# Kernel optimization log

Hardware: AMD Instinct MI355X
Metric: run time of the kernel (lower is better)

Reference implementation:

```python
import jax, jax.numpy as jnp
import numpy as np

EPS = 1e-5  # BatchNorm1d default eps


def gcn_conv(x, src, dst, w, b, n):
    # src/dst already include self-loops. Symmetric normalization D^-1/2 (A+I) D^-1/2.
    deg = jnp.zeros((n,), x.dtype).at[dst].add(1.0)
    dinv = jnp.where(deg > 0, jax.lax.rsqrt(jnp.maximum(deg, 1.0)), 0.0)
    norm = dinv[src] * dinv[dst]                      # [E+N]
    h = x @ w                                          # [B, N, H]
    msg = h[:, src, :] * norm[None, :, None]           # gather + scale  [B, E+N, H]
    agg = jnp.zeros_like(h).at[:, dst, :].add(msg)     # scatter-add
    return agg + b


def batch_norm(h, gamma, beta):
    # training-mode BN over the flattened (B*N) axis, biased variance (torch BN forward)
    mu = h.mean(axis=(0, 1))
    var = ((h - mu) ** 2).mean(axis=(0, 1))
    return (h - mu) * jax.lax.rsqrt(var + EPS) * gamma + beta


def reference(x, edge_index, W1, b1, W2, b2, gamma1, beta1, gamma2, beta2, Wc, bc):
    n = x.shape[1]
    loops = jnp.arange(n)
    src = jnp.concatenate([edge_index[0], loops])
    dst = jnp.concatenate([edge_index[1], loops])
    h = jax.nn.relu(gcn_conv(x, src, dst, W1, b1, n))
    h = batch_norm(h, gamma1, beta1)
    # dropout(p=0.2) treated as identity (eval / deterministic reference)
    h = jax.nn.relu(gcn_conv(h, src, dst, W2, b2, n))
    h = batch_norm(h, gamma2, beta2)
    out = (h @ Wc + bc).squeeze(-1)                    # [B, N]
    return out


def setup_inputs() -> dict:
    key = jax.random.key(0)
    ks = jax.random.split(key, 8)
    B, N, E, F, H = 4, 20000, 320000, 64, 128
    s = lambda fan: 1.0 / np.sqrt(fan)
    return {
        "x": jax.random.normal(ks[0], (B, N, F), dtype=jnp.float32),
        "edge_index": jax.random.randint(ks[1], (2, E), 0, N, dtype=jnp.int64),
        "W1": jax.random.normal(ks[2], (F, H), dtype=jnp.float32) * s(F),
        "b1": jnp.zeros((H,), jnp.float32),
        "W2": jax.random.normal(ks[3], (H, H), dtype=jnp.float32) * s(H),
        "b2": jnp.zeros((H,), jnp.float32),
        "gamma1": jnp.ones((H,), jnp.float32),
        "beta1": jnp.zeros((H,), jnp.float32),
        "gamma2": jnp.ones((H,), jnp.float32),
        "beta2": jnp.zeros((H,), jnp.float32),
        "Wc": jax.random.normal(ks[4], (H, 1), dtype=jnp.float32) * s(H),
        "bc": jnp.zeros((1,), jnp.float32),
    }
```

## Files before the change

kernel.cpp:

```cpp
#include <hip/hip_runtime.h>

constexpr int Bb = 4;
constexpr int Nn = 20000;
constexpr int Ff = 64;
constexpr int Hh = 128;
constexpr float BN_EPS = 1e-5f;
constexpr int NSLOTS = 64;
constexpr int NB = (Nn + 1023) / 1024;

typedef __attribute__((ext_vector_type(8))) short bf16x8;
typedef __attribute__((ext_vector_type(4))) float f32x4;

__device__ inline unsigned f2bf(float f) {
    unsigned u = __float_as_uint(f);
    return (u + 0x7fffu + ((u >> 16) & 1u)) >> 16;
}
__device__ inline unsigned pack2(float lo, float hi) { return f2bf(lo) | (f2bf(hi) << 16); }
__device__ inline float bf_lo(unsigned w) { return __uint_as_float(w << 16); }
__device__ inline float bf_hi(unsigned w) { return __uint_as_float(w & 0xffff0000u); }

template <int NU>
__device__ inline void ldrow(unsigned* u, const unsigned* p) {
    if constexpr (NU == 2) { const uint2 t = *(const uint2*)p; u[0] = t.x; u[1] = t.y; }
    else { const uint4 t = *(const uint4*)p; u[0] = t.x; u[1] = t.y; u[2] = t.z; u[3] = t.w; }
}
template <int NU>
__device__ inline void acc_row(float* a, const unsigned* u, float nm) {
#pragma unroll
    for (int c = 0; c < NU; ++c) {
        a[2 * c]     = fmaf(nm, bf_lo(u[c]), a[2 * c]);
        a[2 * c + 1] = fmaf(nm, bf_hi(u[c]), a[2 * c + 1]);
    }
}

__global__ void k_deg(const int* __restrict__ dst, int E, int* __restrict__ deg) {
    int e = blockIdx.x * blockDim.x + threadIdx.x;
    if (e < E) atomicAdd(&deg[dst[e]], 1);
}

__global__ __launch_bounds__(1024) void k_scan1(const int* __restrict__ deg,
                                                int* __restrict__ rowptr,
                                                int* __restrict__ bsum) {
    __shared__ int wsum[16];
    const int tid = threadIdx.x, lane = tid & 63, wid = tid >> 6;
    const int i = blockIdx.x * 1024 + tid;
    const int cnt = (i < Nn) ? (deg[i] + 1) : 0;
    int v = cnt;
#pragma unroll
    for (int d = 1; d < 64; d <<= 1) {
        const int t = __shfl_up(v, d);
        if (lane >= d) v += t;
    }
    if (lane == 63) wsum[wid] = v;
    __syncthreads();
    if (wid == 0) {
        const int orig = (lane < 16) ? wsum[lane] : 0;
        int w = orig;
#pragma unroll
        for (int d = 1; d < 16; d <<= 1) {
            const int t = __shfl_up(w, d);
            if (lane >= d) w += t;
        }
        if (lane == 15) bsum[blockIdx.x] = w;
        if (lane < 16) wsum[lane] = w - orig;
    }
    __syncthreads();
    if (i < Nn) rowptr[i] = wsum[wid] + (v - cnt);
}

__global__ void k_scan2(int* __restrict__ bsum) {
    const int lane = threadIdx.x;
    const int v = (lane < NB) ? bsum[lane] : 0;
    int s = v;
#pragma unroll
    for (int d = 1; d < 64; d <<= 1) {
        const int t = __shfl_up(s, d);
        if (lane >= d) s += t;
    }
    if (lane < NB) bsum[lane] = s - v;
}

__global__ __launch_bounds__(1024) void k_scan3(const int* __restrict__ deg,
                                                int* __restrict__ rowptr,
                                                const int* __restrict__ bsum,
                                                int* __restrict__ cursor,
                                                float* __restrict__ dinv) {
    const int i = blockIdx.x * 1024 + threadIdx.x;
    if (i >= Nn) return;
    const int cnt = deg[i] + 1;
    const int excl = rowptr[i] + bsum[blockIdx.x];
    rowptr[i] = excl;
    cursor[i] = excl;
    dinv[i] = rsqrtf((float)cnt);
    if (i == Nn - 1) rowptr[Nn] = excl + cnt;
}

__global__ void k_fill(const int* __restrict__ src, const int* __restrict__ dst, int E,
                       const float* __restrict__ dinv, int* __restrict__ cursor,
                       int* __restrict__ csr_src, float* __restrict__ csr_norm,
                       float* __restrict__ nsum) {
    int t = blockIdx.x * blockDim.x + threadIdx.x;
    int s, d;
    if (t < E) { s = src[t]; d = dst[t]; }
    else if (t < E + Nn) { s = d = t - E; }
    else return;
    int pos = atomicAdd(&cursor[d], 1);
    const float nm = dinv[s] * dinv[d];
    csr_src[pos]  = s;
    csr_norm[pos] = nm;
    atomicAdd(&nsum[d], nm);
}

__global__ void k_cvt(const float* __restrict__ x, unsigned* __restrict__ xb) {
    const int t = blockIdx.x * 256 + threadIdx.x;
    if (t >= Bb * Nn * 32) return;
    const int c2 = t & 31;
    const int bn = t >> 5;
    const int n  = bn % Nn;
    const int b  = bn / Nn;
    const float2 v = *(const float2*)&x[(size_t)t * 2];
    xb[((size_t)n * Bb + b) * 32 + c2] = pack2(v.x, v.y);
}

__global__ void k_wt1(const float* __restrict__ W, unsigned short* __restrict__ WTf) {
    const int f = blockIdx.x * 256 + threadIdx.x;
    if (f >= 128 * Ff) return;
    const int j = f & 7, lane = (f >> 3) & 63, rest = f >> 9;
    const int ks = rest & 1, tt = rest >> 1;
    const int col = tt * 16 + (lane & 15);
    const int k = ks * 32 + ((lane >> 4) << 3) + j;
    WTf[f] = (unsigned short)f2bf(W[(size_t)k * 128 + col]);
}

__global__ __launch_bounds__(128) void k_prep2(const float* __restrict__ gsum,
                                               const float* __restrict__ gsq,
                                               const float* __restrict__ gamma,
                                               const float* __restrict__ beta,
                                               const float* __restrict__ W2,
                                               unsigned short* __restrict__ WT2f,
                                               float* __restrict__ shW2) {
    __shared__ float sc_s[128], sh_s[128];
    const int c = threadIdx.x;
    float s = 0.f, q = 0.f;
    for (int j = 0; j < NSLOTS; ++j) { s += gsum[j * 128 + c]; q += gsq[j * 128 + c]; }
    const float inv = 1.0f / (float)(Bb * Nn);
    const float mu  = s * inv;
    const float var = q * inv - mu * mu;
    const float sc  = gamma[c] * rsqrtf(var + BN_EPS);
    sc_s[c] = sc;
    sh_s[c] = beta[c] - mu * sc;
    __syncthreads();
    if (blockIdx.x < 64) {
#pragma unroll
        for (int i = 0; i < 2; ++i) {
            const int f = blockIdx.x * 256 + i * 128 + c;
            const int j = f & 7, lane = (f >> 3) & 63, rest = f >> 9;
            const int ks = rest & 3, tt = rest >> 2;
            const int col = tt * 16 + (lane & 15);
            const int k = ks * 32 + ((lane >> 4) << 3) + j;
            WT2f[f] = (unsigned short)f2bf(sc_s[k] * W2[(size_t)k * 128 + col]);
        }
    } else {
        float a = 0.f;
        for (int k = 0; k < 128; ++k) a = fmaf(sh_s[k], W2[(size_t)k * 128 + c], a);
        shW2[c] = a;
    }
}

template <int K, bool L2E>
__global__ __launch_bounds__(64, 6) void k_fmm(const unsigned* __restrict__ G,
                                               const int* __restrict__ rowptr,
                                               const int* __restrict__ csr_src,
                                               const float* __restrict__ csr_norm,
                                               const unsigned short* __restrict__ WTf,
                                               const float* __restrict__ bias,
                                               const float* __restrict__ nsum,
                                               const float* __restrict__ shW2,
                                               unsigned short* __restrict__ Yout,
                                               float* __restrict__ gsum,
                                               float* __restrict__ gsq) {
    constexpr int NKS = K / 32;
    constexpr int AST = K + 8;
    constexpr int NU = K / 32;
    constexpr int ROWU = Bb * K / 2;
    __shared__ alignas(16) unsigned short sA[16 * AST];

    const int lane = threadIdx.x;
    const int cg = lane & 15, kg = lane >> 4;
    const int g = blockIdx.x;
    const int row0 = g * 16;

#pragma unroll
    for (int j = 0; j < 4; ++j) {
        const int v = g * 4 + j;
        const int beg = rowptr[v], end = rowptr[v + 1];
        float a[2 * NU];
#pragma unroll
        for (int c = 0; c < 2 * NU; ++c) a[c] = 0.f;
        int e = beg;
        for (; e + 8 <= end; e += 8) {
            unsigned u[8][NU];
            int si[8];
#pragma unroll
            for (int q = 0; q < 8; ++q) si[q] = csr_src[e + q];
#pragma unroll
            for (int q = 0; q < 8; ++q)
                ldrow<NU>(u[q], G + (size_t)si[q] * ROWU + lane * NU);
#pragma unroll
            for (int q = 0; q < 8; ++q) acc_row<NU>(a, u[q], csr_norm[e + q]);
        }
        for (; e + 4 <= end; e += 4) {
            unsigned u[4][NU];
            int si[4];
#pragma unroll
            for (int q = 0; q < 4; ++q) si[q] = csr_src[e + q];
#pragma unroll
            for (int q = 0; q < 4; ++q)
                ldrow<NU>(u[q], G + (size_t)si[q] * ROWU + lane * NU);
#pragma unroll
            for (int q = 0; q < 4; ++q) acc_row<NU>(a, u[q], csr_norm[e + q]);
        }
        for (; e < end; ++e) {
            unsigned u[NU];
            ldrow<NU>(u, G + (size_t)csr_src[e] * ROWU + lane * NU);
            acc_row<NU>(a, u, csr_norm[e]);
        }
        const int row = j * 4 + kg;
        unsigned p[NU];
#pragma unroll
        for (int c = 0; c < NU; ++c) p[c] = pack2(a[2 * c], a[2 * c + 1]);
        if constexpr (NU == 2) *(uint2*)&sA[row * AST + cg * 4] = *(const uint2*)p;
        else                   *(uint4*)&sA[row * AST + cg * 8] = *(const uint4*)p;
    }

    f32x4 acc[8];
#pragma unroll
    for (int t = 0; t < 8; ++t) acc[t] = (f32x4){0.f, 0.f, 0.f, 0.f};
#pragma unroll
    for (int ks = 0; ks < NKS; ++ks) {
        const bf16x8 av = *(const bf16x8*)&sA[cg * AST + ks * 32 + kg * 8];
#pragma unroll
        for (int t = 0; t < 8; ++t) {
            const bf16x8 bv = *(const bf16x8*)&WTf[(size_t)((t * NKS + ks) * 64 + lane) * 8];
            acc[t] = __builtin_amdgcn_mfma_f32_16x16x32_bf16(av, bv, acc[t], 0, 0, 0);
        }
    }

    const int rbase = kg * 4;
    float ns = 0.f;
    if (L2E) ns = nsum[g * 4 + kg];
    float* gs = gsum + (size_t)(g & (NSLOTS - 1)) * 128;
    float* gq = gsq  + (size_t)(g & (NSLOTS - 1)) * 128;
#pragma unroll
    for (int t = 0; t < 8; ++t) {
        const int col = t * 16 + cg;
        float badd = bias[col];
        if (L2E) badd = fmaf(ns, shW2[col], badd);
        float s = 0.f, q = 0.f;
#pragma unroll
        for (int jj = 0; jj < 4; ++jj) {
            const float y = fmaxf(acc[t][jj] + badd, 0.f);
            Yout[(size_t)(row0 + rbase + jj) * 128 + col] = (unsigned short)f2bf(y);
            s += y; q = fmaf(y, y, q);
        }
        s += __shfl_xor(s, 16); s += __shfl_xor(s, 32);
        q += __shfl_xor(q, 16); q += __shfl_xor(q, 32);
        if (kg == 0) { atomicAdd(&gs[col], s); atomicAdd(&gq[col], q); }
    }
}

__global__ void k_bnfin2(const float* __restrict__ gsum, const float* __restrict__ gsq,
                         const float* __restrict__ gamma, const float* __restrict__ beta,
                         const float* __restrict__ Wc, const float* __restrict__ bc,
                         float* __restrict__ wcs, float* __restrict__ kc) {
    __shared__ float red[128];
    const int c = threadIdx.x;
    float s = 0.f, q = 0.f;
    for (int j = 0; j < NSLOTS; ++j) { s += gsum[j * 128 + c]; q += gsq[j * 128 + c]; }
    const float inv = 1.0f / (float)(Bb * Nn);
    const float mu  = s * inv;
    const float var = q * inv - mu * mu;
    const float sc  = gamma[c] * rsqrtf(var + BN_EPS);
    const float sh  = beta[c] - mu * sc;
    const float w   = Wc[c];
    wcs[c] = sc * w;
    red[c] = sh * w;
    __syncthreads();
    for (int st = 64; st; st >>= 1) {
        if (c < st) red[c] += red[c + st];
        __syncthreads();
    }
    if (c == 0) kc[0] = red[0] + bc[0];
}

__global__ __launch_bounds__(256) void k_cls(const unsigned* __restrict__ h2,
                                             const float* __restrict__ wcs,
                                             const float* __restrict__ kc,
                                             float* __restrict__ out) {
    const int wave = threadIdx.x >> 6;
    const int lane = threadIdx.x & 63;
    const size_t row = (size_t)blockIdx.x * 4 + wave;
    if (row >= (size_t)Bb * Nn) return;
    const unsigned w = h2[row * 64 + lane];
    const float2 wc = *(const float2*)&wcs[lane * 2];
    float p = bf_lo(w) * wc.x + bf_hi(w) * wc.y;
#pragma unroll
    for (int off = 32; off; off >>= 1) p += __shfl_down(p, off);
    if (lane == 0) {
        const int n = (int)(row >> 2), b = (int)(row & 3);
        out[(size_t)b * Nn + n] = p + kc[0];
    }
}

extern "C" void kernel_launch(void* const* d_in, const int* in_sizes, int n_in,
                              void* d_out, int out_size, void* d_ws, size_t ws_size,
                              hipStream_t stream) {
    const float* x      = (const float*)d_in[0];
    const int*   ei     = (const int*)d_in[1];
    const float* W1     = (const float*)d_in[2];
    const float* b1     = (const float*)d_in[3];
    const float* W2     = (const float*)d_in[4];
    const float* b2     = (const float*)d_in[5];
    const float* gamma1 = (const float*)d_in[6];
    const float* beta1  = (const float*)d_in[7];
    const float* gamma2 = (const float*)d_in[8];
    const float* beta2  = (const float*)d_in[9];
    const float* Wc     = (const float*)d_in[10];
    const float* bc     = (const float*)d_in[11];
    float* out = (float*)d_out;

    const int E = in_sizes[1] / 2;
    const int* src = ei;
    const int* dst = ei + E;

    char* ws = (char*)d_ws;
    size_t off = 0;
    auto alloc = [&](size_t bytes) -> char* {
        char* p = ws + off;
        off += (bytes + 255) & ~(size_t)255;
        return p;
    };
    int*      deg      = (int*)     alloc((size_t)Nn * 4);
    float*    nsum     = (float*)   alloc((size_t)Nn * 4);
    float*    gstat    = (float*)   alloc((size_t)4 * NSLOTS * 128 * 4);
    const size_t zspan = (size_t)((char*)(gstat + 4 * NSLOTS * 128) - (char*)deg);
    float* gsum1 = gstat;
    float* gsq1  = gstat + NSLOTS * 128;
    float* gsum2 = gstat + 2 * NSLOTS * 128;
    float* gsq2  = gstat + 3 * NSLOTS * 128;

    int*      cursor   = (int*)     alloc((size_t)Nn * 4);
    int*      rowptr   = (int*)     alloc((size_t)(Nn + 1) * 4);
    int*      bsum     = (int*)     alloc((size_t)NB * 4);
    float*    dinv     = (float*)   alloc((size_t)Nn * 4);
    int*      csr_src  = (int*)     alloc((size_t)(E + Nn) * 4);
    float*    csr_norm = (float*)   alloc((size_t)(E + Nn) * 4);
    float*    wcs      = (float*)   alloc(128 * 4);
    float*    kc       = (float*)   alloc(256);
    unsigned short* WT1f = (unsigned short*)alloc((size_t)128 * Ff * 2);
    unsigned short* WT2f = (unsigned short*)alloc((size_t)128 * Hh * 2);
    float*          shW2 = (float*)         alloc((size_t)128 * 4);
    unsigned*       xb   = (unsigned*)      alloc((size_t)Nn * Bb * 32 * 4);
    unsigned short* h1b  = (unsigned short*)alloc((size_t)Bb * Nn * Hh * 2);
    unsigned short* h2b  = (unsigned short*)alloc((size_t)Bb * Nn * Hh * 2);

    (void)hipMemsetAsync(deg, 0, zspan, stream);

    k_deg<<<(E + 255) / 256, 256, 0, stream>>>(dst, E, deg);
    k_scan1<<<NB, 1024, 0, stream>>>(deg, rowptr, bsum);
    k_scan2<<<1, 64, 0, stream>>>(bsum);
    k_scan3<<<NB, 1024, 0, stream>>>(deg, rowptr, bsum, cursor, dinv);
    k_fill<<<(E + Nn + 255) / 256, 256, 0, stream>>>(src, dst, E, dinv, cursor,
                                                     csr_src, csr_norm, nsum);
    k_cvt<<<(Bb * Nn * 32 + 255) / 256, 256, 0, stream>>>(x, xb);
    k_wt1<<<(128 * Ff) / 256, 256, 0, stream>>>(W1, WT1f);

    k_fmm<Ff, false><<<Nn / 4, 64, 0, stream>>>(
        xb, rowptr, csr_src, csr_norm, WT1f, b1, nullptr, nullptr, h1b, gsum1, gsq1);
    k_prep2<<<65, 128, 0, stream>>>(gsum1, gsq1, gamma1, beta1, W2, WT2f, shW2);
    k_fmm<Hh, true><<<Nn / 4, 64, 0, stream>>>(
        (const unsigned*)h1b, rowptr, csr_src, csr_norm, WT2f, b2, nsum, shW2,
        h2b, gsum2, gsq2);
    k_bnfin2<<<1, Hh, 0, stream>>>(gsum2, gsq2, gamma2, beta2, Wc, bc, wcs, kc);

    k_cls<<<(Bb * Nn + 3) / 4, 256, 0, stream>>>((const unsigned*)h2b, wcs, kc, out);
}
```

Baseline: 184.2 us.

## Merge preprocessing kernels, single-block scan, halve nodes per fused GCN block

Folds the degree count, x-to-bf16 conversion and W1 transpose into one kernel, and replaces the three-kernel prefix scan with a single-block looping scan. This cuts kernel launch count. The fused gather/matmul kernel now handles 2 nodes per 64-thread block instead of 4, doubling the grid and raising the occupancy hint. The trade-off is that half the MFMA tile rows are padding, wasting matrix work, and the serial scan runs on one block only.

```diff
diff --git a/kernel.cpp b/kernel.cpp
--- a/kernel.cpp
+++ b/kernel.cpp
@@ -6,7 +6,6 @@
 constexpr int Hh = 128;
 constexpr float BN_EPS = 1e-5f;
 constexpr int NSLOTS = 64;
-constexpr int NB = (Nn + 1023) / 1024;
 
 typedef __attribute__((ext_vector_type(8))) short bf16x8;
 typedef __attribute__((ext_vector_type(4))) float f32x4;
@@ -33,66 +32,81 @@
     }
 }
 
-__global__ void k_deg(const int* __restrict__ dst, int E, int* __restrict__ deg) {
-    int e = blockIdx.x * blockDim.x + threadIdx.x;
-    if (e < E) atomicAdd(&deg[dst[e]], 1);
-}
-
-__global__ __launch_bounds__(1024) void k_scan1(const int* __restrict__ deg,
-                                                int* __restrict__ rowptr,
-                                                int* __restrict__ bsum) {
+__global__ __launch_bounds__(256) void k_pre(const int* __restrict__ dst, int E,
+                                             int NDEG,
+                                             int* __restrict__ deg,
+                                             const float* __restrict__ x,
+                                             unsigned* __restrict__ xb,
+                                             const float* __restrict__ W1,
+                                             unsigned short* __restrict__ WTf) {
+    const int b = blockIdx.x;
+    if (b < NDEG) {
+        const int e = b * 256 + threadIdx.x;
+        if (e < E) atomicAdd(&deg[dst[e]], 1);
+    } else if (b < NDEG + (Bb * Nn * 32) / 256) {
+        const int t = (b - NDEG) * 256 + threadIdx.x;
+        const int c2 = t & 31;
+        const int bn = t >> 5;
+        const int n  = bn % Nn;
+        const int bb = bn / Nn;
+        const float2 v = *(const float2*)&x[(size_t)t * 2];
+        xb[((size_t)n * Bb + bb) * 32 + c2] = pack2(v.x, v.y);
+    } else {
+        const int f = (b - NDEG - (Bb * Nn * 32) / 256) * 256 + threadIdx.x;
+        if (f < 128 * Ff) {
+            const int j = f & 7, lane = (f >> 3) & 63, rest = f >> 9;
+            const int ks = rest & 1, tt = rest >> 1;
+            const int col = tt * 16 + (lane & 15);
+            const int k = ks * 32 + ((lane >> 4) << 3) + j;
+            WTf[f] = (unsigned short)f2bf(W1[(size_t)k * 128 + col]);
+        }
+    }
+}
+
+__global__ __launch_bounds__(1024) void k_scan(const int* __restrict__ deg,
+                                               int* __restrict__ rowptr,
+                                               int* __restrict__ cursor,
+                                               float* __restrict__ dinv) {
     __shared__ int wsum[16];
-    const int tid = threadIdx.x, lane = tid & 63, wid = tid >> 6;
-    const int i = blockIdx.x * 1024 + tid;
-    const int cnt = (i < Nn) ? (deg[i] + 1) : 0;
-    int v = cnt;
-#pragma unroll
-    for (int d = 1; d < 64; d <<= 1) {
-        const int t = __shfl_up(v, d);
-        if (lane >= d) v += t;
-    }
-    if (lane == 63) wsum[wid] = v;
+    __shared__ int carry_s, tsum_s;
+    const int tid = threadIdx.x;
+    const int lane = tid & 63, wid = tid >> 6;
+    if (tid == 0) carry_s = 0;
     __syncthreads();
-    if (wid == 0) {
-        const int orig = (lane < 16) ? wsum[lane] : 0;
-        int w = orig;
-#pragma unroll
-        for (int d = 1; d < 16; d <<= 1) {
-            const int t = __shfl_up(w, d);
-            if (lane >= d) w += t;
-        }
-        if (lane == 15) bsum[blockIdx.x] = w;
-        if (lane < 16) wsum[lane] = w - orig;
-    }
-    __syncthreads();
-    if (i < Nn) rowptr[i] = wsum[wid] + (v - cnt);
-}
-
-__global__ void k_scan2(int* __restrict__ bsum) {
-    const int lane = threadIdx.x;
-    const int v = (lane < NB) ? bsum[lane] : 0;
-    int s = v;
-#pragma unroll
-    for (int d = 1; d < 64; d <<= 1) {
-        const int t = __shfl_up(s, d);
-        if (lane >= d) s += t;
-    }
-    if (lane < NB) bsum[lane] = s - v;
-}
-
-__global__ __launch_bounds__(1024) void k_scan3(const int* __restrict__ deg,
-                                                int* __restrict__ rowptr,
-                                                const int* __restrict__ bsum,
-                                                int* __restrict__ cursor,
-                                                float* __restrict__ dinv) {
-    const int i = blockIdx.x * 1024 + threadIdx.x;
-    if (i >= Nn) return;
-    const int cnt = deg[i] + 1;
-    const int excl = rowptr[i] + bsum[blockIdx.x];
-    rowptr[i] = excl;
-    cursor[i] = excl;
-    dinv[i] = rsqrtf((float)cnt);
-    if (i == Nn - 1) rowptr[Nn] = excl + cnt;
+    for (int base = 0; base < Nn; base += 1024) {
+        const int i = base + tid;
+        const int cnt = (i < Nn) ? (deg[i] + 1) : 0;
+        int v = cnt;
+#pragma unroll
+        for (int d = 1; d < 64; d <<= 1) {
+            const int t = __shfl_up(v, d);
+            if (lane >= d) v += t;
+        }
+        if (lane == 63) wsum[wid] = v;
+        __syncthreads();
+        if (wid == 0) {
+            const int orig = (lane < 16) ? wsum[lane] : 0;
+            int w = orig;
+#pragma unroll
+            for (int d = 1; d < 16; d <<= 1) {
+                const int t = __shfl_up(w, d);
+                if (lane >= d) w += t;
+            }
+            if (lane == 15) tsum_s = w;
+            if (lane < 16) wsum[lane] = w - orig;
+        }
+        __syncthreads();
+        const int c = carry_s;
+        const int excl = c + wsum[wid] + (v - cnt);
+        if (i < Nn) {
+            rowptr[i] = excl;
+            cursor[i] = excl;
+            dinv[i]   = rsqrtf((float)cnt);
+        }
+        __syncthreads();
+        if (tid == 0) carry_s += tsum_s;
+    }
+    if (tid == 0) rowptr[Nn] = carry_s;
 }
 
 __global__ void k_fill(const int* __restrict__ src, const int* __restrict__ dst, int E,
@@ -109,27 +123,6 @@
     csr_src[pos]  = s;
     csr_norm[pos] = nm;
     atomicAdd(&nsum[d], nm);
-}
-
-__global__ void k_cvt(const float* __restrict__ x, unsigned* __restrict__ xb) {
-    const int t = blockIdx.x * 256 + threadIdx.x;
-    if (t >= Bb * Nn * 32) return;
-    const int c2 = t & 31;
-    const int bn = t >> 5;
-    const int n  = bn % Nn;
-    const int b  = bn / Nn;
-    const float2 v = *(const float2*)&x[(size_t)t * 2];
-    xb[((size_t)n * Bb + b) * 32 + c2] = pack2(v.x, v.y);
-}
-
-__global__ void k_wt1(const float* __restrict__ W, unsigned short* __restrict__ WTf) {
-    const int f = blockIdx.x * 256 + threadIdx.x;
-    if (f >= 128 * Ff) return;
-    const int j = f & 7, lane = (f >> 3) & 63, rest = f >> 9;
-    const int ks = rest & 1, tt = rest >> 1;
-    const int col = tt * 16 + (lane & 15);
-    const int k = ks * 32 + ((lane >> 4) << 3) + j;
-    WTf[f] = (unsigned short)f2bf(W[(size_t)k * 128 + col]);
 }
 
 __global__ __launch_bounds__(128) void k_prep2(const float* __restrict__ gsum,
@@ -168,7 +161,7 @@
 }
 
 template <int K, bool L2E>
-__global__ __launch_bounds__(64, 6) void k_fmm(const unsigned* __restrict__ G,
+__global__ __launch_bounds__(64, 8) void k_fmm(const unsigned* __restrict__ G,
                                                const int* __restrict__ rowptr,
                                                const int* __restrict__ csr_src,
                                                const float* __restrict__ csr_norm,
@@ -188,11 +181,11 @@
     const int lane = threadIdx.x;
     const int cg = lane & 15, kg = lane >> 4;
     const int g = blockIdx.x;
-    const int row0 = g * 16;
-
-#pragma unroll
-    for (int j = 0; j < 4; ++j) {
-        const int v = g * 4 + j;
+    const int row0 = g * 8;
+
+#pragma unroll
+    for (int j = 0; j < 2; ++j) {
+        const int v = g * 2 + j;
         const int beg = rowptr[v], end = rowptr[v + 1];
         float a[2 * NU];
 #pragma unroll
@@ -248,20 +241,22 @@
 
     const int rbase = kg * 4;
     float ns = 0.f;
-    if (L2E) ns = nsum[g * 4 + kg];
+    if (L2E) ns = nsum[g * 2 + (kg & 1)];
     float* gs = gsum + (size_t)(g & (NSLOTS - 1)) * 128;
     float* gq = gsq  + (size_t)(g & (NSLOTS - 1)) * 128;
 #pragma unroll
     for (int t = 0; t < 8; ++t) {
         const int col = t * 16 + cg;
-        float badd = bias[col];
-        if (L2E) badd = fmaf(ns, shW2[col], badd);
         float s = 0.f, q = 0.f;
-#pragma unroll
-        for (int jj = 0; jj < 4; ++jj) {
-            const float y = fmaxf(acc[t][jj] + badd, 0.f);
-            Yout[(size_t)(row0 + rbase + jj) * 128 + col] = (unsigned short)f2bf(y);
-            s += y; q = fmaf(y, y, q);
+        if (kg < 2) {
+            float badd = bias[col];
+            if (L2E) badd = fmaf(ns, shW2[col], badd);
+#pragma unroll
+            for (int jj = 0; jj < 4; ++jj) {
+                const float y = fmaxf(acc[t][jj] + badd, 0.f);
+                Yout[(size_t)(row0 + rbase + jj) * 128 + col] = (unsigned short)f2bf(y);
+                s += y; q = fmaf(y, y, q);
+            }
         }
         s += __shfl_xor(s, 16); s += __shfl_xor(s, 32);
         q += __shfl_xor(q, 16); q += __shfl_xor(q, 32);
@@ -351,7 +346,6 @@
 
     int*      cursor   = (int*)     alloc((size_t)Nn * 4);
     int*      rowptr   = (int*)     alloc((size_t)(Nn + 1) * 4);
-    int*      bsum     = (int*)     alloc((size_t)NB * 4);
     float*    dinv     = (float*)   alloc((size_t)Nn * 4);
     int*      csr_src  = (int*)     alloc((size_t)(E + Nn) * 4);
     float*    csr_norm = (float*)   alloc((size_t)(E + Nn) * 4);
@@ -366,19 +360,17 @@
 
     (void)hipMemsetAsync(deg, 0, zspan, stream);
 
-    k_deg<<<(E + 255) / 256, 256, 0, stream>>>(dst, E, deg);
-    k_scan1<<<NB, 1024, 0, stream>>>(deg, rowptr, bsum);
-    k_scan2<<<1, 64, 0, stream>>>(bsum);
-    k_scan3<<<NB, 1024, 0, stream>>>(deg, rowptr, bsum, cursor, dinv);
+    const int NDEG = (E + 255) / 256;
+    const int NCVT = (Bb * Nn * 32) / 256;
+    k_pre<<<NDEG + NCVT + 32, 256, 0, stream>>>(dst, E, NDEG, deg, x, xb, W1, WT1f);
+    k_scan<<<1, 1024, 0, stream>>>(deg, rowptr, cursor, dinv);
     k_fill<<<(E + Nn + 255) / 256, 256, 0, stream>>>(src, dst, E, dinv, cursor,
                                                      csr_src, csr_norm, nsum);
-    k_cvt<<<(Bb * Nn * 32 + 255) / 256, 256, 0, stream>>>(x, xb);
-    k_wt1<<<(128 * Ff) / 256, 256, 0, stream>>>(W1, WT1f);
-
-    k_fmm<Ff, false><<<Nn / 4, 64, 0, stream>>>(
+
+    k_fmm<Ff, false><<<Nn / 2, 64, 0, stream>>>(
         xb, rowptr, csr_src, csr_norm, WT1f, b1, nullptr, nullptr, h1b, gsum1, gsq1);
     k_prep2<<<65, 128, 0, stream>>>(gsum1, gsq1, gamma1, beta1, W2, WT2f, shW2);
-    k_fmm<Hh, true><<<Nn / 4, 64, 0, stream>>>(
+    k_fmm<Hh, true><<<Nn / 2, 64, 0, stream>>>(
         (const unsigned*)h1b, rowptr, csr_src, csr_norm, WT2f, b2, nsum, shW2,
         h2b, gsum2, gsq2);
     k_bnfin2<<<1, Hh, 0, stream>>>(gsum2, gsq2, gamma2, beta2, Wc, bc, wcs, kc);
```

Measured after the change: 228.9 us. +24.2%, slower.
